# Kernel optimization log

Hardware: AMD Instinct MI355X
Metric: run time of the kernel (lower is better)

The kernel has to match this reference:

```python
import jax, jax.numpy as jnp
import numpy as np

B, N, E = 4, 4096, 65536
FIN, FOUT = 128, 64
ALPHA = 0.2          # LeakyReLU negative slope
NEG = -9e15          # mask value from original code


def setup_inputs() -> dict:
    key = jax.random.key(0)
    k1, k2, k3, k4 = jax.random.split(key, 4)
    h = jax.random.normal(k1, (B, N, FIN), dtype=jnp.float32)
    edge_index = jax.random.randint(k2, (B, 2, E), 0, N, dtype=jnp.int32)
    # Xavier-uniform-like params
    W = jax.random.uniform(k3, (FIN, FOUT), jnp.float32, -1.0, 1.0) * (1.414 * np.sqrt(6.0 / (FIN + FOUT)))
    a = jax.random.uniform(k4, (2 * FOUT, 1), jnp.float32, -1.0, 1.0) * (1.414 * np.sqrt(6.0 / (2 * FOUT + 1)))
    return {"h": h, "edge_index": edge_index, "W": W, "a": a}


def reference(h, edge_index, W, a):
    # Wh: [B, N, FOUT]
    Wh = jnp.einsum('bnf,fo->bno', h, W)
    Wh_flat = Wh.reshape(-1, FOUT)  # [B*N, FOUT]

    # Faithful to original: raw node ids (< N) index the flattened tensor,
    # i.e. edge features are gathered from batch 0's rows.
    src = edge_index[:, 0].reshape(-1)  # [B*E]
    tgt = edge_index[:, 1].reshape(-1)  # [B*E]
    a_input = jnp.concatenate([Wh_flat[src], Wh_flat[tgt]], axis=1)  # [B*E, 2*FOUT]
    e = (a_input @ a)[:, 0]  # [B*E]

    b_idx = jnp.repeat(jnp.arange(B), E)
    e_dense = jnp.zeros((B, N, N), e.dtype).at[b_idx, src, tgt].set(e)
    e_dense = jax.nn.leaky_relu(e_dense, ALPHA)

    attention = jnp.where(e_dense > 0, e_dense, NEG)
    attention = jax.nn.softmax(attention, axis=1)  # softmax over dim=1 as in original
    # dropout p=0.0 -> no-op

    h_prime = jnp.einsum('bmn,bnf->bmf', attention, Wh)  # [B, N, FOUT]
    return jax.nn.elu(h_prime)  # concat=True path
```

## Files before the change

### kernel.cpp

```cpp
#include <hip/hip_runtime.h>
#include <hip/hip_bf16.h>

#define BB 4
#define NN 4096
#define EE 65536
#define FIN 128
#define FOUT 64
#define CAP 64

__device__ __forceinline__ unsigned enc_f32(float f) {
    unsigned b = __float_as_uint(f);
    return (b & 0x80000000u) ? ~b : (b | 0x80000000u);
}
__device__ __forceinline__ float dec_f32(unsigned e) {
    unsigned b = (e & 0x80000000u) ? (e & 0x7FFFFFFFu) : ~e;
    return __uint_as_float(b);
}

__global__ __launch_bounds__(256) void wh_kernel(const float* __restrict__ h,
                                                 const float* __restrict__ W,
                                                 float* __restrict__ Wh) {
    __shared__ float hs[32][132];
    __shared__ float Ws[128][64];
    int tid = threadIdx.x;
    long row0 = (long)blockIdx.x * 32;
    for (int i = tid; i < 2048; i += 256) {
        float4 v = ((const float4*)W)[i];
        int k = (i * 4) >> 6, c = (i * 4) & 63;
        *(float4*)&Ws[k][c] = v;
    }
    for (int i = tid; i < 1024; i += 256) {
        float4 v = ((const float4*)(h + row0 * FIN))[i];
        int r = (i * 4) >> 7, c = (i * 4) & 127;
        *(float4*)&hs[r][c] = v;
    }
    __syncthreads();
    int tx = tid & 15, ty = tid >> 4;
    int c0 = tx * 4, r0 = ty * 2;
    float acc[2][4] = {};
#pragma unroll
    for (int k = 0; k < 128; k += 4) {
        float4 w0 = *(const float4*)&Ws[k][c0];
        float4 w1 = *(const float4*)&Ws[k + 1][c0];
        float4 w2 = *(const float4*)&Ws[k + 2][c0];
        float4 w3 = *(const float4*)&Ws[k + 3][c0];
#pragma unroll
        for (int r = 0; r < 2; ++r) {
            float4 hv = *(const float4*)&hs[r0 + r][k];
            acc[r][0] += hv.x * w0.x + hv.y * w1.x + hv.z * w2.x + hv.w * w3.x;
            acc[r][1] += hv.x * w0.y + hv.y * w1.y + hv.z * w2.y + hv.w * w3.y;
            acc[r][2] += hv.x * w0.z + hv.y * w1.z + hv.z * w2.z + hv.w * w3.z;
            acc[r][3] += hv.x * w0.w + hv.y * w1.w + hv.z * w2.w + hv.w * w3.w;
        }
    }
#pragma unroll
    for (int r = 0; r < 2; ++r)
        *(float4*)&Wh[(row0 + r0 + r) * FOUT + c0] = *(float4*)&acc[r][0];
}

__global__ void attn_coef_kernel(const float* __restrict__ Wh, const float* __restrict__ a,
                                 float* __restrict__ as_, float* __restrict__ at_) {
    int tid = threadIdx.x;
    int f = tid & 63, w = tid >> 6;
    int n = blockIdx.x * 4 + w;
    float v = Wh[(long)n * FOUT + f];
    float ps = v * a[f];
    float pt = v * a[64 + f];
    for (int off = 32; off; off >>= 1) {
        ps += __shfl_down(ps, off);
        pt += __shfl_down(pt, off);
    }
    if (f == 0) { as_[n] = ps; at_[n] = pt; }
}

__global__ void edge_kernel(const int* __restrict__ ei, const float* __restrict__ as_,
                            const float* __restrict__ at_, unsigned* __restrict__ bitmap,
                            unsigned* __restrict__ Menc, int* __restrict__ deg,
                            int* __restrict__ csr) {
    int idx = blockIdx.x * 256 + threadIdx.x;
    int b = idx >> 16;
    int j = idx & 65535;
    const int* eb = ei + (long)b * 2 * EE;
    int s = eb[j], t = eb[EE + j];
    float as_s = as_[s];
    float e = as_s + at_[t];
    if (e > 0.f) {
        int row = (b << 12) | s;
        long bit = ((long)row << 12) | t;
        unsigned m = 1u << (t & 31);
        unsigned old = atomicOr(&bitmap[bit >> 5], m);
        if (!(old & m)) {
            atomicMax(&Menc[(b << 12) | t], enc_f32(as_s));
            int slot = atomicAdd(&deg[row], 1);
            if (slot < CAP) csr[row * CAP + slot] = t;
        }
    }
}

__global__ void denom_kernel(const int* __restrict__ deg, const int* __restrict__ csr,
                             const float* __restrict__ as_, const unsigned* __restrict__ Menc,
                             float* __restrict__ D) {
    int tid = threadIdx.x;
    int lane = tid & 63;
    int row = blockIdx.x * 4 + (tid >> 6);
    int b = row >> 12, s = row & 4095;
    int d = min(deg[row], CAP);
    float as_s = as_[s];
    for (int j = lane; j < d; j += 64) {
        int t = csr[row * CAP + j];
        float M = dec_f32(Menc[(b << 12) | t]);
        atomicAdd(&D[(b << 12) | t], expf(as_s - M));
    }
}

__global__ void gcoef_kernel(const unsigned* __restrict__ Menc, const float* __restrict__ D,
                             float* __restrict__ g) {
    int i = blockIdx.x * 256 + threadIdx.x;
    unsigned m = Menc[i];
    g[i] = m ? expf(-dec_f32(m)) / D[i] : 0.f;
}

__global__ void base_kernel(const unsigned* __restrict__ Menc, const float* __restrict__ Wh,
                            float* __restrict__ base) {
    int bx = blockIdx.x;
    int b = bx >> 5, chunk = bx & 31;
    int f = threadIdx.x & 63, ty = threadIdx.x >> 6;
    float acc = 0.f;
    int t0 = chunk * (NN / 32);
    for (int t = t0 + ty; t < t0 + NN / 32; t += 4)
        if (Menc[(b << 12) | t] == 0u) acc += Wh[(((long)b << 12) | t) * FOUT + f];
    __shared__ float red[4][64];
    red[ty][f] = acc;
    __syncthreads();
    if (ty == 0)
        atomicAdd(&base[(b << 6) | f],
                  (red[0][f] + red[1][f] + red[2][f] + red[3][f]) * (1.0f / NN));
}

__global__ void gather_kernel(const int* __restrict__ deg, const int* __restrict__ csr,
                              const float* __restrict__ as_, const float* __restrict__ g,
                              const float* __restrict__ Wh, const float* __restrict__ base,
                              float* __restrict__ out) {
    int tid = threadIdx.x;
    int lane = tid & 63;
    int row = blockIdx.x * 4 + (tid >> 6);
    int b = row >> 12, s = row & 4095;
    int d = min(deg[row], CAP);
    float Es = expf(as_[s]);
    float acc = 0.f;
    const int* cr = csr + row * CAP;
    const float* Whb = Wh + (((long)b << 12) * FOUT);
    for (int j = 0; j < d; ++j) {
        int t = cr[j];
        float w = g[(b << 12) | t];
        acc += w * Whb[t * FOUT + lane];
    }
    float x = Es * acc + base[(b << 6) | lane];
    out[(long)row * FOUT + lane] = x > 0.f ? x : expm1f(x);
}

extern "C" void kernel_launch(void* const* d_in, const int* in_sizes, int n_in,
                              void* d_out, int out_size, void* d_ws, size_t ws_size,
                              hipStream_t stream) {
    const float* h  = (const float*)d_in[0];
    const int*   ei = (const int*)d_in[1];
    const float* W  = (const float*)d_in[2];
    const float* a  = (const float*)d_in[3];
    float* out = (float*)d_out;

    char* ws = (char*)d_ws;
    float*    Wh     = (float*)(ws);
    unsigned* bitmap = (unsigned*)(ws + 4194304);
    int*      csr    = (int*)(ws + 12582912);
    int*      deg    = (int*)(ws + 16777216);
    unsigned* Menc   = (unsigned*)(ws + 16842752);
    float*    D      = (float*)(ws + 16908288);
    float*    g      = (float*)(ws + 16973824);
    float*    as_    = (float*)(ws + 17039360);
    float*    at_    = (float*)(ws + 17055744);
    float*    base   = (float*)(ws + 17072128);

    hipMemsetAsync(bitmap, 0, 8388608, stream);
    hipMemsetAsync(deg, 0, 65536 * 3, stream);
    hipMemsetAsync(base, 0, BB * FOUT * sizeof(float), stream);

    wh_kernel<<<BB * NN / 32, 256, 0, stream>>>(h, W, Wh);
    attn_coef_kernel<<<NN / 4, 256, 0, stream>>>(Wh, a, as_, at_);
    edge_kernel<<<(BB * EE) / 256, 256, 0, stream>>>(ei, as_, at_, bitmap, Menc, deg, csr);
    denom_kernel<<<(BB * NN) / 4, 256, 0, stream>>>(deg, csr, as_, Menc, D);
    gcoef_kernel<<<(BB * NN) / 256, 256, 0, stream>>>(Menc, D, g);
    base_kernel<<<BB * 32, 256, 0, stream>>>(Menc, Wh, base);
    gather_kernel<<<(BB * NN) / 4, 256, 0, stream>>>(deg, csr, as_, g, Wh, base, out);
}
```

Before: 88.45 us.

## Drop bitmap dedup, dedupe CSR in-wave, precompute W·a for attention scores

Removes the 8 MB bitmap and its memset, moving duplicate-edge removal into a per-row wave ballot inside the denominator kernel. Attention coefficients are now computed from h·(W·a), with W·a precomputed in a new init kernel, so they no longer wait on Wh. The init kernel also replaces the memsets, and the gcoef kernel is folded into the gather kernel. The risk is that duplicates now consume CSR slots before dedup, so rows with more than CAP raw edges could drop unique neighbours. The gather also recomputes exp per edge.

Measured after the change: 79.47 us. -10.2%, faster.

```diff
diff --git a/kernel.cpp b/kernel.cpp
--- a/kernel.cpp
+++ b/kernel.cpp
@@ -15,6 +15,43 @@
 __device__ __forceinline__ float dec_f32(unsigned e) {
     unsigned b = (e & 0x80000000u) ? (e & 0x7FFFFFFFu) : ~e;
     return __uint_as_float(b);
+}
+
+__global__ void init_kernel(const float* __restrict__ W, const float* __restrict__ a,
+                            int* __restrict__ deg, unsigned* __restrict__ Menc,
+                            float* __restrict__ D, float* __restrict__ base,
+                            float* __restrict__ Wa) {
+    int tid = threadIdx.x;
+    int gid = blockIdx.x * 256 + tid;
+    deg[gid] = 0;
+    Menc[gid] = 0u;
+    D[gid] = 0.f;
+    if (gid < BB * FOUT) base[gid] = 0.f;
+    if (blockIdx.x == 0) {
+        int half = tid >> 7, k = tid & 127;
+        const float* wr = W + k * FOUT;
+        const float* av = a + half * FOUT;
+        float s = 0.f;
+#pragma unroll 16
+        for (int f = 0; f < FOUT; ++f) s += wr[f] * av[f];
+        Wa[half * 128 + k] = s;
+    }
+}
+
+__global__ void as_at_kernel(const float* __restrict__ h, const float* __restrict__ Wa,
+                             float* __restrict__ as_, float* __restrict__ at_) {
+    int tid = threadIdx.x;
+    int lane = tid & 63;
+    int n = blockIdx.x * 4 + (tid >> 6);
+    float h0v = h[(long)n * FIN + lane];
+    float h1v = h[(long)n * FIN + 64 + lane];
+    float ps = h0v * Wa[lane] + h1v * Wa[64 + lane];
+    float pt = h0v * Wa[128 + lane] + h1v * Wa[192 + lane];
+    for (int off = 32; off; off >>= 1) {
+        ps += __shfl_down(ps, off);
+        pt += __shfl_down(pt, off);
+    }
+    if (lane == 0) { as_[n] = ps; at_[n] = pt; }
 }
 
 __global__ __launch_bounds__(256) void wh_kernel(const float* __restrict__ h,
@@ -58,25 +95,9 @@
         *(float4*)&Wh[(row0 + r0 + r) * FOUT + c0] = *(float4*)&acc[r][0];
 }
 
-__global__ void attn_coef_kernel(const float* __restrict__ Wh, const float* __restrict__ a,
-                                 float* __restrict__ as_, float* __restrict__ at_) {
-    int tid = threadIdx.x;
-    int f = tid & 63, w = tid >> 6;
-    int n = blockIdx.x * 4 + w;
-    float v = Wh[(long)n * FOUT + f];
-    float ps = v * a[f];
-    float pt = v * a[64 + f];
-    for (int off = 32; off; off >>= 1) {
-        ps += __shfl_down(ps, off);
-        pt += __shfl_down(pt, off);
-    }
-    if (f == 0) { as_[n] = ps; at_[n] = pt; }
-}
-
 __global__ void edge_kernel(const int* __restrict__ ei, const float* __restrict__ as_,
-                            const float* __restrict__ at_, unsigned* __restrict__ bitmap,
-                            unsigned* __restrict__ Menc, int* __restrict__ deg,
-                            int* __restrict__ csr) {
+                            const float* __restrict__ at_, unsigned* __restrict__ Menc,
+                            int* __restrict__ deg, int* __restrict__ csr) {
     int idx = blockIdx.x * 256 + threadIdx.x;
     int b = idx >> 16;
     int j = idx & 65535;
@@ -86,38 +107,37 @@
     float e = as_s + at_[t];
     if (e > 0.f) {
         int row = (b << 12) | s;
-        long bit = ((long)row << 12) | t;
-        unsigned m = 1u << (t & 31);
-        unsigned old = atomicOr(&bitmap[bit >> 5], m);
-        if (!(old & m)) {
-            atomicMax(&Menc[(b << 12) | t], enc_f32(as_s));
-            int slot = atomicAdd(&deg[row], 1);
-            if (slot < CAP) csr[row * CAP + slot] = t;
-        }
-    }
-}
-
-__global__ void denom_kernel(const int* __restrict__ deg, const int* __restrict__ csr,
-                             const float* __restrict__ as_, const unsigned* __restrict__ Menc,
-                             float* __restrict__ D) {
+        atomicMax(&Menc[(b << 12) | t], enc_f32(as_s));
+        int slot = atomicAdd(&deg[row], 1);
+        if (slot < CAP) csr[row * CAP + slot] = t;
+    }
+}
+
+__global__ void dedup_denom_kernel(int* __restrict__ deg, int* __restrict__ csr,
+                                   const float* __restrict__ as_,
+                                   const unsigned* __restrict__ Menc,
+                                   float* __restrict__ D) {
     int tid = threadIdx.x;
     int lane = tid & 63;
     int row = blockIdx.x * 4 + (tid >> 6);
     int b = row >> 12, s = row & 4095;
-    int d = min(deg[row], CAP);
-    float as_s = as_[s];
-    for (int j = lane; j < d; j += 64) {
-        int t = csr[row * CAP + j];
+    int draw = min(deg[row], CAP);
+    int t = -1;
+    if (lane < draw) t = csr[row * CAP + lane];
+    bool dup = false;
+    for (int k = 0; k < draw; ++k) {
+        int tk = __shfl(t, k);
+        if (k < lane && tk == t) dup = true;
+    }
+    bool keep = (lane < draw) && !dup;
+    unsigned long long mask = __ballot(keep);
+    int pfx = __popcll(mask & ((1ull << lane) - 1ull));
+    if (keep) {
+        csr[row * CAP + pfx] = t;
         float M = dec_f32(Menc[(b << 12) | t]);
-        atomicAdd(&D[(b << 12) | t], expf(as_s - M));
-    }
-}
-
-__global__ void gcoef_kernel(const unsigned* __restrict__ Menc, const float* __restrict__ D,
-                             float* __restrict__ g) {
-    int i = blockIdx.x * 256 + threadIdx.x;
-    unsigned m = Menc[i];
-    g[i] = m ? expf(-dec_f32(m)) / D[i] : 0.f;
+        atomicAdd(&D[(b << 12) | t], expf(as_[s] - M));
+    }
+    if (lane == 0) deg[row] = __popcll(mask);
 }
 
 __global__ void base_kernel(const unsigned* __restrict__ Menc, const float* __restrict__ Wh,
@@ -138,24 +158,25 @@
 }
 
 __global__ void gather_kernel(const int* __restrict__ deg, const int* __restrict__ csr,
-                              const float* __restrict__ as_, const float* __restrict__ g,
-                              const float* __restrict__ Wh, const float* __restrict__ base,
-                              float* __restrict__ out) {
+                              const float* __restrict__ as_, const unsigned* __restrict__ Menc,
+                              const float* __restrict__ D, const float* __restrict__ Wh,
+                              const float* __restrict__ base, float* __restrict__ out) {
     int tid = threadIdx.x;
     int lane = tid & 63;
     int row = blockIdx.x * 4 + (tid >> 6);
     int b = row >> 12, s = row & 4095;
-    int d = min(deg[row], CAP);
-    float Es = expf(as_[s]);
+    int d = deg[row];
+    float as_s = as_[s];
     float acc = 0.f;
     const int* cr = csr + row * CAP;
     const float* Whb = Wh + (((long)b << 12) * FOUT);
     for (int j = 0; j < d; ++j) {
         int t = cr[j];
-        float w = g[(b << 12) | t];
+        float M = dec_f32(Menc[(b << 12) | t]);
+        float w = expf(as_s - M) / D[(b << 12) | t];
         acc += w * Whb[t * FOUT + lane];
     }
-    float x = Es * acc + base[(b << 6) | lane];
+    float x = acc + base[(b << 6) | lane];
     out[(long)row * FOUT + lane] = x > 0.f ? x : expm1f(x);
 }
 
@@ -169,26 +190,21 @@
     float* out = (float*)d_out;
 
     char* ws = (char*)d_ws;
-    float*    Wh     = (float*)(ws);
-    unsigned* bitmap = (unsigned*)(ws + 4194304);
-    int*      csr    = (int*)(ws + 12582912);
-    int*      deg    = (int*)(ws + 16777216);
-    unsigned* Menc   = (unsigned*)(ws + 16842752);
-    float*    D      = (float*)(ws + 16908288);
-    float*    g      = (float*)(ws + 16973824);
-    float*    as_    = (float*)(ws + 17039360);
-    float*    at_    = (float*)(ws + 17055744);
-    float*    base   = (float*)(ws + 17072128);
-
-    hipMemsetAsync(bitmap, 0, 8388608, stream);
-    hipMemsetAsync(deg, 0, 65536 * 3, stream);
-    hipMemsetAsync(base, 0, BB * FOUT * sizeof(float), stream);
-
+    float*    Wh   = (float*)(ws);
+    int*      csr  = (int*)(ws + 4194304);
+    int*      deg  = (int*)(ws + 8388608);
+    unsigned* Menc = (unsigned*)(ws + 8454144);
+    float*    D    = (float*)(ws + 8519680);
+    float*    as_  = (float*)(ws + 8585216);
+    float*    at_  = (float*)(ws + 8601600);
+    float*    base = (float*)(ws + 8617984);
+    float*    Wa   = (float*)(ws + 8619008);
+
+    init_kernel<<<64, 256, 0, stream>>>(W, a, deg, Menc, D, base, Wa);
     wh_kernel<<<BB * NN / 32, 256, 0, stream>>>(h, W, Wh);
-    attn_coef_kernel<<<NN / 4, 256, 0, stream>>>(Wh, a, as_, at_);
-    edge_kernel<<<(BB * EE) / 256, 256, 0, stream>>>(ei, as_, at_, bitmap, Menc, deg, csr);
-    denom_kernel<<<(BB * NN) / 4, 256, 0, stream>>>(deg, csr, as_, Menc, D);
-    gcoef_kernel<<<(BB * NN) / 256, 256, 0, stream>>>(Menc, D, g);
+    as_at_kernel<<<NN / 4, 256, 0, stream>>>(h, Wa, as_, at_);
+    edge_kernel<<<(BB * EE) / 256, 256, 0, stream>>>(ei, as_, at_, Menc, deg, csr);
+    dedup_denom_kernel<<<(BB * NN) / 4, 256, 0, stream>>>(deg, csr, as_, Menc, D);
     base_kernel<<<BB * 32, 256, 0, stream>>>(Menc, Wh, base);
-    gather_kernel<<<(BB * NN) / 4, 256, 0, stream>>>(deg, csr, as_, g, Wh, base, out);
-}
+    gather_kernel<<<(BB * NN) / 4, 256, 0, stream>>>(deg, csr, as_, Menc, D, Wh, base, out);
+}
```
